# Optimization experiments

Hardware: AMD Instinct MI355X
Metric: run time of the kernel (lower is better)

The kernel has to match this reference:

```python
import jax, jax.numpy as jnp
import numpy as np

N, B, M = 262144, 4, 32
C3D, C2D, MID, OUT = 64, 256, 128, 64
H, W = 96, 312
VOXEL_SIZE = jnp.array([0.05, 0.05, 0.1], dtype=jnp.float32)
PC_RANGE = jnp.array([0.0, -40.0, -3.0], dtype=jnp.float32)
CLASS_W3D = jnp.array([0.85, 0.95, 0.6], dtype=jnp.float32)  # Car, Pedestrian, Cyclist
DEFAULT_W3D = 0.8
EPS = 1e-5

def _bn(x, g, b, m, v):
    # eval-mode batchnorm
    return (x - m) * jax.lax.rsqrt(v + EPS) * g + b

def setup_inputs():
    key = jax.random.key(0)
    ks = jax.random.split(key, 16)
    vb = jax.random.randint(ks[0], (N,), 0, B)
    vz = jax.random.randint(ks[1], (N,), 0, 40)
    vy = jax.random.randint(ks[2], (N,), 0, 1600)
    vx = jax.random.randint(ks[3], (N,), 0, 1408)
    voxel_coords = jnp.stack([vb, vz, vy, vx], axis=1).astype(jnp.int32)
    voxel_features = jax.random.normal(ks[4], (N, C3D), dtype=jnp.float32)
    image_features = jax.random.normal(ks[5], (B, C2D, H, W), dtype=jnp.float32)
    cxy = jax.random.uniform(ks[6], (B, M, 2)) * jnp.array([70.4, 80.0]) + jnp.array([0.0, -40.0])
    cz = jax.random.uniform(ks[7], (B, M, 1)) * 4.0 - 3.0
    dims = jax.random.uniform(ks[8], (B, M, 3)) * 3.0 + 1.0
    yaw = jax.random.uniform(ks[9], (B, M, 1)) * 6.28
    gt_boxes = jnp.concatenate([cxy, cz, dims, yaw], axis=-1).astype(jnp.float32)
    gt_classes = jax.random.randint(ks[10], (B, M), 0, 3)
    def lin(k, o, i):
        return (jax.random.normal(k, (o, i), dtype=jnp.float32) / np.float32(np.sqrt(i)))
    return dict(
        voxel_features=voxel_features, voxel_coords=voxel_coords,
        image_features=image_features, gt_boxes=gt_boxes, gt_classes=gt_classes,
        w_vt=lin(ks[11], MID, C3D), b_vt=jnp.zeros(MID),
        g_vt=jnp.ones(MID), be_vt=jnp.zeros(MID), m_vt=jnp.zeros(MID), v_vt=jnp.ones(MID),
        w_it=lin(ks[12], MID, C2D), b_it=jnp.zeros(MID),
        g_it=jnp.ones(MID), be_it=jnp.zeros(MID), m_it=jnp.zeros(MID), v_it=jnp.ones(MID),
        w_f=lin(ks[13], OUT, 2 * MID), b_f=jnp.zeros(OUT),
        g_f=jnp.ones(OUT), be_f=jnp.zeros(OUT), m_f=jnp.zeros(OUT), v_f=jnp.ones(OUT),
    )

def reference(voxel_features, voxel_coords, image_features, gt_boxes, gt_classes,
              w_vt, b_vt, g_vt, be_vt, m_vt, v_vt,
              w_it, b_it, g_it, be_it, m_it, v_it,
              w_f, b_f, g_f, be_f, m_f, v_f):
    b_idx = voxel_coords[:, 0]
    xyz = jnp.stack([voxel_coords[:, 3], voxel_coords[:, 2], voxel_coords[:, 1]], axis=1).astype(jnp.float32)
    centers_raw = xyz * VOXEL_SIZE + PC_RANGE            # class-aware path (no half-voxel offset)
    centers = centers_raw + VOXEL_SIZE * 0.5             # sampling path

    # voxel transform: Linear + BN + ReLU
    vt = jax.nn.relu(_bn(voxel_features @ w_vt.T + b_vt, g_vt, be_vt, m_vt, v_vt))

    # image transform: 1x1 conv + BN + ReLU over all images at once
    it = jnp.einsum('oc,bchw->bohw', w_it, image_features) + b_it[None, :, None, None]
    it = jax.nn.relu(_bn(it, g_it[None, :, None, None], be_it[None, :, None, None],
                         m_it[None, :, None, None], v_it[None, :, None, None]))

    # fallback projection (no calib): xy*10 + [W/2, H/2], normalize to [-1,1], clamp
    px = centers[:, 0] * 10.0 + W / 2.0
    py = centers[:, 1] * 10.0 + H / 2.0
    nx = jnp.clip(px / W * 2.0 - 1.0, -1.0, 1.0)
    ny = jnp.clip(py / H * 2.0 - 1.0, -1.0, 1.0)
    # grid_sample bilinear, align_corners=False, zero padding
    fx = ((nx + 1.0) * W - 1.0) * 0.5
    fy = ((ny + 1.0) * H - 1.0) * 0.5
    x0 = jnp.floor(fx); y0 = jnp.floor(fy)

    def gather(xi, yi):
        valid = (xi >= 0) & (xi < W) & (yi >= 0) & (yi < H)
        xc = jnp.clip(xi, 0, W - 1).astype(jnp.int32)
        yc = jnp.clip(yi, 0, H - 1).astype(jnp.int32)
        return it[b_idx, :, yc, xc] * valid[:, None].astype(it.dtype)  # (N, MID)

    wx1 = (fx - x0)[:, None]; wy1 = (fy - y0)[:, None]
    sampled = (gather(x0, y0) * (1.0 - wx1) * (1.0 - wy1)
             + gather(x0 + 1, y0) * wx1 * (1.0 - wy1)
             + gather(x0, y0 + 1) * (1.0 - wx1) * wy1
             + gather(x0 + 1, y0 + 1) * wx1 * wy1)

    # class-aware weights: axis-aligned point-in-box test; later boxes overwrite earlier
    cen = gt_boxes[..., :3][b_idx]          # (N, M, 3)
    dim = gt_boxes[..., 3:6][b_idx]         # (N, M, 3)
    valid_box = (gt_boxes[..., 3] > 0)[b_idx]  # (N, M)
    inb = jnp.all(jnp.abs(centers_raw[:, None, :] - cen) < dim * 0.5, axis=-1) & valid_box
    any_in = jnp.any(inb, axis=1)
    last = jnp.argmax(jnp.where(inb, jnp.arange(M), -1), axis=1)  # last matching box
    cls = gt_classes[b_idx, last]
    w3d = jnp.where(any_in, CLASS_W3D[cls], DEFAULT_W3D)[:, None]

    fused = jnp.concatenate([vt * w3d, sampled * (1.0 - w3d)], axis=1)
    out = jax.nn.relu(_bn(fused @ w_f.T + b_f, g_f, be_f, m_f, v_f))
    return out
```

## Files before the change

kernel.cpp:

```cpp
#include <hip/hip_runtime.h>

typedef _Float16 half8  __attribute__((ext_vector_type(8)));
typedef _Float16 half4v __attribute__((ext_vector_type(4)));
typedef _Float16 half2v __attribute__((ext_vector_type(2)));
typedef float    f32x4  __attribute__((ext_vector_type(4)));

#define N_VOX  262144
#define BATCH  4
#define NBOX   32
#define C3D_   64
#define C2D_   256
#define MIDC   128
#define OUTC   64
#define IH     96
#define IW     312
#define IHW    (IH*IW)
#define EPSF   1e-5f

#define MFMA16(a,b,c) __builtin_amdgcn_mfma_f32_16x16x32_f16(a,b,c,0,0,0)

__global__ __launch_bounds__(256) void prep_all(
    const int*   __restrict__ coords,
    const float* __restrict__ gtb,
    const int*   __restrict__ gtc,
    const float* __restrict__ w_vt, const float* __restrict__ g_vt,
    const float* __restrict__ v_vt, const float* __restrict__ b_vt,
    const float* __restrict__ be_vt, const float* __restrict__ m_vt,
    const float* __restrict__ w_it, const float* __restrict__ g_it,
    const float* __restrict__ v_it, const float* __restrict__ b_it,
    const float* __restrict__ be_it, const float* __restrict__ m_it,
    const float* __restrict__ w_f, const float* __restrict__ g_f,
    const float* __restrict__ v_f, const float* __restrict__ b_f,
    const float* __restrict__ be_f, const float* __restrict__ m_f,
    _Float16* __restrict__ w_vt_s, _Float16* __restrict__ w_it_s,
    _Float16* __restrict__ w_f1_s, _Float16* __restrict__ w_f2_s,
    float* __restrict__ sb_vt, float* __restrict__ sb_it,
    float* __restrict__ sb_f,  float* __restrict__ w3d_buf)
{
    __shared__ float s_box[BATCH*NBOX*7];
    __shared__ int   s_cls[BATCH*NBOX];
    const int tid = threadIdx.x;
    for (int i = tid; i < BATCH*NBOX*7; i += 256) s_box[i] = gtb[i];
    for (int i = tid; i < BATCH*NBOX;   i += 256) s_cls[i] = gtc[i];
    __syncthreads();

    const int v = blockIdx.x * 256 + tid;

    {
        const int4 cc = ((const int4*)coords)[v];
        const int vb = cc.x;
        const float crx = cc.w * 0.05f;
        const float cry = cc.z * 0.05f - 40.0f;
        const float crz = cc.y * 0.1f  - 3.0f;
        const float* gb = s_box + vb*(NBOX*7);
        int lastm = -1;
        #pragma unroll 8
        for (int m = 0; m < NBOX; ++m) {
            float dx = gb[m*7+3];
            bool in = (fabsf(crx - gb[m*7+0]) < dx * 0.5f) &&
                      (fabsf(cry - gb[m*7+1]) < gb[m*7+4] * 0.5f) &&
                      (fabsf(crz - gb[m*7+2]) < gb[m*7+5] * 0.5f) &&
                      (dx > 0.f);
            if (in) lastm = m;
        }
        float w3 = 0.8f;
        if (lastm >= 0) {
            int cls = s_cls[vb*NBOX + lastm];
            w3 = (cls == 0) ? 0.85f : ((cls == 1) ? 0.95f : 0.6f);
        }
        w3d_buf[v] = w3;
    }

    if (v < MIDC*C3D_) {
        int o = v >> 6;
        float sa = g_vt[o] * rsqrtf(v_vt[o] + EPSF);
        w_vt_s[v] = (_Float16)(w_vt[v] * sa);
    }
    if (v < MIDC*C2D_) {
        int o = v >> 8;
        float sa = g_it[o] * rsqrtf(v_it[o] + EPSF);
        w_it_s[v] = (_Float16)(w_it[v] * sa);
    }
    if (v < OUTC*C2D_) {
        int o = v >> 8, k = v & 255;
        float sa = g_f[o] * rsqrtf(v_f[o] + EPSF);
        float val = w_f[v] * sa;
        if (k < 128) w_f1_s[o*128 + k]       = (_Float16)val;
        else         w_f2_s[o*128 + (k-128)] = (_Float16)val;
    }
    if (v < MIDC) {
        float sa = g_vt[v] * rsqrtf(v_vt[v] + EPSF);
        sb_vt[v] = (b_vt[v] - m_vt[v]) * sa + be_vt[v];
        float si = g_it[v] * rsqrtf(v_it[v] + EPSF);
        sb_it[v] = (b_it[v] - m_it[v]) * si + be_it[v];
    }
    if (v < OUTC) {
        float sa = g_f[v] * rsqrtf(v_f[v] + EPSF);
        sb_f[v] = (b_f[v] - m_f[v]) * sa + be_f[v];
    }
}

__global__ __launch_bounds__(256, 4) void img_transform(
    const float* __restrict__ img,
    const _Float16* __restrict__ w_it_s,
    const _Float16* __restrict__ w_f2_s,
    const float* __restrict__ sb_it,
    _Float16* __restrict__ Jout)
{
    __shared__ __align__(16) _Float16 s_mem[64*136];

    const int p0   = blockIdx.x * 64;
    const int b    = blockIdx.y;
    const int tid  = threadIdx.x;
    const int lane = tid & 63;
    const int wv   = tid >> 6;
    const int r    = lane & 15;
    const int kh   = lane >> 4;

    f32x4 acc[4][2] = {};

    const int p  = tid & 63;
    const int cb = (tid >> 6) * 2;

    const float sbit0 = sb_it[wv*32 + r];
    const float sbit1 = sb_it[wv*32 + 16 + r];

    for (int kc = 0; kc < 4; ++kc) {
        #pragma unroll
        for (int i = 0; i < 8; ++i) {
            int c = cb + i*8;
            float x0 = img[(size_t)(b*C2D_ + kc*64 + c    )*IHW + p0 + p];
            float x1 = img[(size_t)(b*C2D_ + kc*64 + c + 1)*IHW + p0 + p];
            half2v h; h[0] = (_Float16)x0; h[1] = (_Float16)x1;
            *(half2v*)&s_mem[p*72 + c] = h;
        }
        half8 bw[2][2];
        #pragma unroll
        for (int nt = 0; nt < 2; ++nt)
            #pragma unroll
            for (int ks = 0; ks < 2; ++ks) {
                int o = wv*32 + nt*16 + r;
                bw[nt][ks] = *(const half8*)&w_it_s[o*C2D_ + kc*64 + ks*32 + kh*8];
            }
        __syncthreads();
        #pragma unroll
        for (int mt = 0; mt < 4; ++mt)
            #pragma unroll
            for (int ks = 0; ks < 2; ++ks) {
                half8 af = *(const half8*)&s_mem[(mt*16 + r)*72 + ks*32 + kh*8];
                acc[mt][0] = MFMA16(af, bw[0][ks], acc[mt][0]);
                acc[mt][1] = MFMA16(af, bw[1][ks], acc[mt][1]);
            }
        __syncthreads();
    }

    #pragma unroll
    for (int nt = 0; nt < 2; ++nt) {
        int o = wv*32 + nt*16 + r;
        float sb = nt ? sbit1 : sbit0;
        #pragma unroll
        for (int mt = 0; mt < 4; ++mt)
            #pragma unroll
            for (int rr = 0; rr < 4; ++rr) {
                int p2 = mt*16 + kh*4 + rr;
                s_mem[p2*136 + o] = (_Float16)fmaxf(acc[mt][nt][rr] + sb, 0.f);
            }
    }
    __syncthreads();

    {
        const int o2 = wv*16 + r;
        half8 bf2[4];
        #pragma unroll
        for (int ks = 0; ks < 4; ++ks)
            bf2[ks] = *(const half8*)&w_f2_s[o2*128 + ks*32 + kh*8];
        #pragma unroll
        for (int mt = 0; mt < 4; ++mt) {
            f32x4 a2 = {0.f,0.f,0.f,0.f};
            #pragma unroll
            for (int ks = 0; ks < 4; ++ks) {
                half8 af = *(const half8*)&s_mem[(mt*16 + r)*136 + ks*32 + kh*8];
                a2 = MFMA16(af, bf2[ks], a2);
            }
            #pragma unroll
            for (int rr = 0; rr < 4; ++rr) {
                int p2 = mt*16 + kh*4 + rr;
                Jout[(size_t)(b*IHW + p0 + p2)*OUTC + o2] = (_Float16)a2[rr];
            }
        }
    }
}

__global__ __launch_bounds__(256, 3) void voxel_fuse(
    const float* __restrict__ vf,
    const int*   __restrict__ coords,
    const _Float16* __restrict__ w_vt_s,
    const float* __restrict__ sb_vt,
    const _Float16* __restrict__ Jimg,
    const _Float16* __restrict__ w_f1_s,
    const float* __restrict__ sb_f,
    const float* __restrict__ w3d_buf,
    float* __restrict__ out)
{
    __shared__ __align__(16) _Float16 s_vf[64*72];
    __shared__ __align__(16) _Float16 s_fused[64*136];
    __shared__ __align__(16) _Float16 s_j[64*72];
    __shared__ float s_w3d[64];

    const int tid  = threadIdx.x;
    const int lane = tid & 63;
    const int wv   = tid >> 6;
    const int v0   = blockIdx.x * 64;
    const int r    = lane & 15;
    const int kh   = lane >> 4;
    const int vsv  = tid >> 2;
    const int q_   = tid & 3;

    float4 vfr[4];
    {
        const float4* src = (const float4*)(vf + (size_t)(v0 + vsv)*C3D_ + q_*16);
        #pragma unroll
        for (int i = 0; i < 4; ++i) vfr[i] = src[i];
    }
    const float w3 = w3d_buf[v0 + vsv];
    const int4 cc = ((const int4*)coords)[v0 + vsv];

    int ga[4]; float gw[4];
    {
        const int vb = cc.x;
        const float crx = cc.w * 0.05f;
        const float cry = cc.z * 0.05f - 40.0f;
        const float px = (crx + 0.025f) * 10.f + 156.f;
        const float py = (cry + 0.025f) * 10.f + 48.f;
        const float nx = fminf(fmaxf(px / 312.f * 2.f - 1.f, -1.f), 1.f);
        const float ny = fminf(fmaxf(py / 96.f  * 2.f - 1.f, -1.f), 1.f);
        const float fx = ((nx + 1.f) * 312.f - 1.f) * 0.5f;
        const float fy = ((ny + 1.f) * 96.f  - 1.f) * 0.5f;
        const float x0f = floorf(fx), y0f = floorf(fy);
        const float wx1 = fx - x0f, wy1 = fy - y0f;
        const int x0 = (int)x0f, y0 = (int)y0f;
        #pragma unroll
        for (int c = 0; c < 4; ++c) {
            int xi = x0 + (c & 1), yi = y0 + (c >> 1);
            bool valid = (xi >= 0) && (xi < IW) && (yi >= 0) && (yi < IH);
            int xc = min(max(xi, 0), IW - 1);
            int yc = min(max(yi, 0), IH - 1);
            ga[c] = ((vb*IH + yc)*IW + xc) * OUTC;
            float wx = (c & 1) ? wx1 : 1.f - wx1;
            float wy = (c >> 1) ? wy1 : 1.f - wy1;
            gw[c] = valid ? wx * wy : 0.f;
        }
    }

    half8 jreg[4][2];
    #pragma unroll
    for (int c = 0; c < 4; ++c)
        #pragma unroll
        for (int h = 0; h < 2; ++h)
            jreg[c][h] = *(const half8*)&Jimg[ga[c] + (h*4 + q_)*8];

    half8 bvt[2][2];
    float sbvt[2];
    #pragma unroll
    for (int nt = 0; nt < 2; ++nt) {
        int o = (2*wv + nt)*16 + r;
        #pragma unroll
        for (int ks = 0; ks < 2; ++ks)
            bvt[nt][ks] = *(const half8*)&w_vt_s[o*C3D_ + ks*32 + kh*8];
        sbvt[nt] = sb_vt[o];
    }
    const int of = wv*16 + r;
    half8 bf1[4];
    #pragma unroll
    for (int ks = 0; ks < 4; ++ks)
        bf1[ks] = *(const half8*)&w_f1_s[of*128 + ks*32 + kh*8];
    const float sbf = sb_f[of];

    #pragma unroll
    for (int i = 0; i < 4; ++i) {
        float4 x = vfr[i];
        half4v h;
        h[0] = (_Float16)x.x; h[1] = (_Float16)x.y;
        h[2] = (_Float16)x.z; h[3] = (_Float16)x.w;
        *(half4v*)&s_vf[vsv*72 + q_*16 + i*4] = h;
    }
    if (q_ == 0) s_w3d[vsv] = w3;
    __syncthreads();

    #pragma unroll
    for (int mt = 0; mt < 4; ++mt) {
        f32x4 a0 = {0.f,0.f,0.f,0.f}, a1 = {0.f,0.f,0.f,0.f};
        #pragma unroll
        for (int ks = 0; ks < 2; ++ks) {
            half8 af = *(const half8*)&s_vf[(mt*16 + r)*72 + ks*32 + kh*8];
            a0 = MFMA16(af, bvt[0][ks], a0);
            a1 = MFMA16(af, bvt[1][ks], a1);
        }
        #pragma unroll
        for (int rr = 0; rr < 4; ++rr) {
            int v = mt*16 + kh*4 + rr;
            float w3v = s_w3d[v];
            s_fused[v*136 + (2*wv+0)*16 + r] =
                (_Float16)(fmaxf(a0[rr] + sbvt[0], 0.f) * w3v);
            s_fused[v*136 + (2*wv+1)*16 + r] =
                (_Float16)(fmaxf(a1[rr] + sbvt[1], 0.f) * w3v);
        }
    }

    {
        float invw = 1.f - w3;
        #pragma unroll
        for (int h = 0; h < 2; ++h) {
            half8 res;
            #pragma unroll
            for (int i = 0; i < 8; ++i) {
                float s = gw[0]*(float)jreg[0][h][i] + gw[1]*(float)jreg[1][h][i]
                        + gw[2]*(float)jreg[2][h][i] + gw[3]*(float)jreg[3][h][i];
                res[i] = (_Float16)(s * invw);
            }
            *(half8*)&s_j[vsv*72 + (h*4 + q_)*8] = res;
        }
    }
    __syncthreads();

    #pragma unroll
    for (int mt = 0; mt < 4; ++mt) {
        f32x4 acc = {0.f,0.f,0.f,0.f};
        #pragma unroll
        for (int ks = 0; ks < 4; ++ks) {
            half8 af = *(const half8*)&s_fused[(mt*16 + r)*136 + ks*32 + kh*8];
            acc = MFMA16(af, bf1[ks], acc);
        }
        #pragma unroll
        for (int rr = 0; rr < 4; ++rr) {
            int v = mt*16 + kh*4 + rr;
            float jv = (float)s_j[v*72 + of];
            out[(size_t)(v0 + v)*OUTC + of] = fmaxf(acc[rr] + jv + sbf, 0.f);
        }
    }
}

extern "C" void kernel_launch(void* const* d_in, const int* in_sizes, int n_in,
                              void* d_out, int out_size, void* d_ws, size_t ws_size,
                              hipStream_t stream)
{
    const float* vf    = (const float*)d_in[0];
    const int*   vc    = (const int*)  d_in[1];
    const float* img   = (const float*)d_in[2];
    const float* gtb   = (const float*)d_in[3];
    const int*   gtc   = (const int*)  d_in[4];
    const float* w_vt  = (const float*)d_in[5];
    const float* b_vt  = (const float*)d_in[6];
    const float* g_vt  = (const float*)d_in[7];
    const float* be_vt = (const float*)d_in[8];
    const float* m_vt  = (const float*)d_in[9];
    const float* v_vt  = (const float*)d_in[10];
    const float* w_it  = (const float*)d_in[11];
    const float* b_it  = (const float*)d_in[12];
    const float* g_it  = (const float*)d_in[13];
    const float* be_it = (const float*)d_in[14];
    const float* m_it  = (const float*)d_in[15];
    const float* v_it  = (const float*)d_in[16];
    const float* w_f   = (const float*)d_in[17];
    const float* b_f   = (const float*)d_in[18];
    const float* g_f   = (const float*)d_in[19];
    const float* be_f  = (const float*)d_in[20];
    const float* m_f   = (const float*)d_in[21];
    const float* v_f   = (const float*)d_in[22];

    _Float16* ws_h   = (_Float16*)d_ws;
    _Float16* Jbuf   = ws_h;
    _Float16* w_vt_s = ws_h + (size_t)BATCH*IHW*OUTC;
    _Float16* w_it_s = w_vt_s + MIDC*C3D_;
    _Float16* w_f1_s = w_it_s + MIDC*C2D_;
    _Float16* w_f2_s = w_f1_s + OUTC*128;
    float*    fbase  = (float*)(w_f2_s + OUTC*128);
    float* sb_vt   = fbase;
    float* sb_it   = sb_vt + MIDC;
    float* sb_f    = sb_it + MIDC;
    float* w3d_buf = sb_f + OUTC;
    float* outp = (float*)d_out;

    prep_all<<<N_VOX/256, 256, 0, stream>>>(
        vc, gtb, gtc,
        w_vt, g_vt, v_vt, b_vt, be_vt, m_vt,
        w_it, g_it, v_it, b_it, be_it, m_it,
        w_f,  g_f,  v_f,  b_f,  be_f,  m_f,
        w_vt_s, w_it_s, w_f1_s, w_f2_s,
        sb_vt, sb_it, sb_f, w3d_buf);

    img_transform<<<dim3(IHW/64, BATCH), 256, 0, stream>>>(
        img, w_it_s, w_f2_s, sb_it, Jbuf);

    voxel_fuse<<<N_VOX/64, 256, 0, stream>>>(
        vf, vc, w_vt_s, sb_vt, Jbuf, w_f1_s, sb_f, w3d_buf, outp);
}
```

Before: 84.82 us.

## Process two voxel tiles per block, prefetching the second tile's inputs

Each block now handles 128 voxels as two 64-voxel tiles. The weights are loaded once and reused across both tiles. The second tile's voxel features, coords and gathered image rows are issued while the first tile's GEMMs run, to hide global-memory and gather latency. The trade-off is higher register pressure and lowered launch bounds (2 instead of 3 blocks), plus half as many blocks in the grid, which can reduce occupancy and latency hiding.

```diff
diff --git a/kernel.cpp b/kernel.cpp
--- a/kernel.cpp
+++ b/kernel.cpp
@@ -191,7 +191,7 @@
     }
 }
 
-__global__ __launch_bounds__(256, 3) void voxel_fuse(
+__global__ __launch_bounds__(256, 2) void voxel_fuse(
     const float* __restrict__ vf,
     const int*   __restrict__ coords,
     const _Float16* __restrict__ w_vt_s,
@@ -210,26 +210,43 @@
     const int tid  = threadIdx.x;
     const int lane = tid & 63;
     const int wv   = tid >> 6;
-    const int v0   = blockIdx.x * 64;
+    const int v0   = blockIdx.x * 128;
     const int r    = lane & 15;
     const int kh   = lane >> 4;
     const int vsv  = tid >> 2;
     const int q_   = tid & 3;
 
-    float4 vfr[4];
+    half8 bvt[2][2];
+    float sbvt[2];
+    #pragma unroll
+    for (int nt = 0; nt < 2; ++nt) {
+        int o = (2*wv + nt)*16 + r;
+        #pragma unroll
+        for (int ks = 0; ks < 2; ++ks)
+            bvt[nt][ks] = *(const half8*)&w_vt_s[o*C3D_ + ks*32 + kh*8];
+        sbvt[nt] = sb_vt[o];
+    }
+    const int of = wv*16 + r;
+    half8 bf1[4];
+    #pragma unroll
+    for (int ks = 0; ks < 4; ++ks)
+        bf1[ks] = *(const half8*)&w_f1_s[of*128 + ks*32 + kh*8];
+    const float sbf = sb_f[of];
+
+    float4 vfrA[4];
     {
         const float4* src = (const float4*)(vf + (size_t)(v0 + vsv)*C3D_ + q_*16);
         #pragma unroll
-        for (int i = 0; i < 4; ++i) vfr[i] = src[i];
-    }
-    const float w3 = w3d_buf[v0 + vsv];
-    const int4 cc = ((const int4*)coords)[v0 + vsv];
-
-    int ga[4]; float gw[4];
-    {
-        const int vb = cc.x;
-        const float crx = cc.w * 0.05f;
-        const float cry = cc.z * 0.05f - 40.0f;
+        for (int i = 0; i < 4; ++i) vfrA[i] = src[i];
+    }
+    const float w3A = w3d_buf[v0 + vsv];
+    const int4  ccA = ((const int4*)coords)[v0 + vsv];
+
+    int gaA[4]; float gwA[4];
+    {
+        const int vb = ccA.x;
+        const float crx = ccA.w * 0.05f;
+        const float cry = ccA.z * 0.05f - 40.0f;
         const float px = (crx + 0.025f) * 10.f + 156.f;
         const float py = (cry + 0.025f) * 10.f + 48.f;
         const float nx = fminf(fmaxf(px / 312.f * 2.f - 1.f, -1.f), 1.f);
@@ -245,47 +262,38 @@
             bool valid = (xi >= 0) && (xi < IW) && (yi >= 0) && (yi < IH);
             int xc = min(max(xi, 0), IW - 1);
             int yc = min(max(yi, 0), IH - 1);
-            ga[c] = ((vb*IH + yc)*IW + xc) * OUTC;
+            gaA[c] = ((vb*IH + yc)*IW + xc) * OUTC;
             float wx = (c & 1) ? wx1 : 1.f - wx1;
             float wy = (c >> 1) ? wy1 : 1.f - wy1;
-            gw[c] = valid ? wx * wy : 0.f;
-        }
-    }
-
-    half8 jreg[4][2];
+            gwA[c] = valid ? wx * wy : 0.f;
+        }
+    }
+    half8 jregA[4][2];
     #pragma unroll
     for (int c = 0; c < 4; ++c)
         #pragma unroll
         for (int h = 0; h < 2; ++h)
-            jreg[c][h] = *(const half8*)&Jimg[ga[c] + (h*4 + q_)*8];
-
-    half8 bvt[2][2];
-    float sbvt[2];
-    #pragma unroll
-    for (int nt = 0; nt < 2; ++nt) {
-        int o = (2*wv + nt)*16 + r;
-        #pragma unroll
-        for (int ks = 0; ks < 2; ++ks)
-            bvt[nt][ks] = *(const half8*)&w_vt_s[o*C3D_ + ks*32 + kh*8];
-        sbvt[nt] = sb_vt[o];
-    }
-    const int of = wv*16 + r;
-    half8 bf1[4];
-    #pragma unroll
-    for (int ks = 0; ks < 4; ++ks)
-        bf1[ks] = *(const half8*)&w_f1_s[of*128 + ks*32 + kh*8];
-    const float sbf = sb_f[of];
+            jregA[c][h] = *(const half8*)&Jimg[gaA[c] + (h*4 + q_)*8];
 
     #pragma unroll
     for (int i = 0; i < 4; ++i) {
-        float4 x = vfr[i];
+        float4 x = vfrA[i];
         half4v h;
         h[0] = (_Float16)x.x; h[1] = (_Float16)x.y;
         h[2] = (_Float16)x.z; h[3] = (_Float16)x.w;
         *(half4v*)&s_vf[vsv*72 + q_*16 + i*4] = h;
     }
-    if (q_ == 0) s_w3d[vsv] = w3;
+    if (q_ == 0) s_w3d[vsv] = w3A;
     __syncthreads();
+
+    float4 vfrB[4];
+    {
+        const float4* src = (const float4*)(vf + (size_t)(v0 + 64 + vsv)*C3D_ + q_*16);
+        #pragma unroll
+        for (int i = 0; i < 4; ++i) vfrB[i] = src[i];
+    }
+    const float w3B = w3d_buf[v0 + 64 + vsv];
+    const int4  ccB = ((const int4*)coords)[v0 + 64 + vsv];
 
     #pragma unroll
     for (int mt = 0; mt < 4; ++mt) {
@@ -308,19 +316,53 @@
     }
 
     {
-        float invw = 1.f - w3;
+        float invw = 1.f - w3A;
         #pragma unroll
         for (int h = 0; h < 2; ++h) {
             half8 res;
             #pragma unroll
             for (int i = 0; i < 8; ++i) {
-                float s = gw[0]*(float)jreg[0][h][i] + gw[1]*(float)jreg[1][h][i]
-                        + gw[2]*(float)jreg[2][h][i] + gw[3]*(float)jreg[3][h][i];
+                float s = gwA[0]*(float)jregA[0][h][i] + gwA[1]*(float)jregA[1][h][i]
+                        + gwA[2]*(float)jregA[2][h][i] + gwA[3]*(float)jregA[3][h][i];
                 res[i] = (_Float16)(s * invw);
             }
             *(half8*)&s_j[vsv*72 + (h*4 + q_)*8] = res;
         }
     }
+
+    int gaB[4]; float gwB[4];
+    {
+        const int vb = ccB.x;
+        const float crx = ccB.w * 0.05f;
+        const float cry = ccB.z * 0.05f - 40.0f;
+        const float px = (crx + 0.025f) * 10.f + 156.f;
+        const float py = (cry + 0.025f) * 10.f + 48.f;
+        const float nx = fminf(fmaxf(px / 312.f * 2.f - 1.f, -1.f), 1.f);
+        const float ny = fminf(fmaxf(py / 96.f  * 2.f - 1.f, -1.f), 1.f);
+        const float fx = ((nx + 1.f) * 312.f - 1.f) * 0.5f;
+        const float fy = ((ny + 1.f) * 96.f  - 1.f) * 0.5f;
+        const float x0f = floorf(fx), y0f = floorf(fy);
+        const float wx1 = fx - x0f, wy1 = fy - y0f;
+        const int x0 = (int)x0f, y0 = (int)y0f;
+        #pragma unroll
+        for (int c = 0; c < 4; ++c) {
+            int xi = x0 + (c & 1), yi = y0 + (c >> 1);
+            bool valid = (xi >= 0) && (xi < IW) && (yi >= 0) && (yi < IH);
+            int xc = min(max(xi, 0), IW - 1);
+            int yc = min(max(yi, 0), IH - 1);
+            gaB[c] = ((vb*IH + yc)*IW + xc) * OUTC;
+            float wx = (c & 1) ? wx1 : 1.f - wx1;
+            float wy = (c >> 1) ? wy1 : 1.f - wy1;
+            gwB[c] = valid ? wx * wy : 0.f;
+        }
+    }
+    half8 jregB[4][2];
+    #pragma unroll
+    for (int c = 0; c < 4; ++c)
+        #pragma unroll
+        for (int h = 0; h < 2; ++h)
+            jregB[c][h] = *(const half8*)&Jimg[gaB[c] + (h*4 + q_)*8];
+
     __syncthreads();
 
     #pragma unroll
@@ -336,6 +378,69 @@
             int v = mt*16 + kh*4 + rr;
             float jv = (float)s_j[v*72 + of];
             out[(size_t)(v0 + v)*OUTC + of] = fmaxf(acc[rr] + jv + sbf, 0.f);
+        }
+    }
+
+    #pragma unroll
+    for (int i = 0; i < 4; ++i) {
+        float4 x = vfrB[i];
+        half4v h;
+        h[0] = (_Float16)x.x; h[1] = (_Float16)x.y;
+        h[2] = (_Float16)x.z; h[3] = (_Float16)x.w;
+        *(half4v*)&s_vf[vsv*72 + q_*16 + i*4] = h;
+    }
+    if (q_ == 0) s_w3d[vsv] = w3B;
+    __syncthreads();
+
+    #pragma unroll
+    for (int mt = 0; mt < 4; ++mt) {
+        f32x4 a0 = {0.f,0.f,0.f,0.f}, a1 = {0.f,0.f,0.f,0.f};
+        #pragma unroll
+        for (int ks = 0; ks < 2; ++ks) {
+            half8 af = *(const half8*)&s_vf[(mt*16 + r)*72 + ks*32 + kh*8];
+            a0 = MFMA16(af, bvt[0][ks], a0);
+            a1 = MFMA16(af, bvt[1][ks], a1);
+        }
+        #pragma unroll
+        for (int rr = 0; rr < 4; ++rr) {
+            int v = mt*16 + kh*4 + rr;
+            float w3v = s_w3d[v];
+            s_fused[v*136 + (2*wv+0)*16 + r] =
+                (_Float16)(fmaxf(a0[rr] + sbvt[0], 0.f) * w3v);
+            s_fused[v*136 + (2*wv+1)*16 + r] =
+                (_Float16)(fmaxf(a1[rr] + sbvt[1], 0.f) * w3v);
+        }
+    }
+
+    {
+        float invw = 1.f - w3B;
+        #pragma unroll
+        for (int h = 0; h < 2; ++h) {
+            half8 res;
+            #pragma unroll
+            for (int i = 0; i < 8; ++i) {
+                float s = gwB[0]*(float)jregB[0][h][i] + gwB[1]*(float)jregB[1][h][i]
+                        + gwB[2]*(float)jregB[2][h][i] + gwB[3]*(float)jregB[3][h][i];
+                res[i] = (_Float16)(s * invw);
+            }
+            *(half8*)&s_j[vsv*72 + (h*4 + q_)*8] = res;
+        }
+    }
+    __syncthreads();
+
+    #pragma unroll
+    for (int mt = 0; mt < 4; ++mt) {
+        f32x4 acc = {0.f,0.f,0.f,0.f};
+        #pragma unroll
+        for (int ks = 0; ks < 4; ++ks) {
+            half8 af = *(const half8*)&s_fused[(mt*16 + r)*136 + ks*32 + kh*8];
+            acc = MFMA16(af, bf1[ks], acc);
+        }
+        #pragma unroll
+        for (int rr = 0; rr < 4; ++rr) {
+            int v = mt*16 + kh*4 + rr;
+            float jv = (float)s_j[v*72 + of];
+            out[(size_t)(v0 + 64 + v)*OUTC + of] = fmaxf(acc[rr] + jv + sbf, 0.f);
         }
     }
 }
@@ -392,6 +497,6 @@
     img_transform<<<dim3(IHW/64, BATCH), 256, 0, stream>>>(
         img, w_it_s, w_f2_s, sb_it, Jbuf);
 
-    voxel_fuse<<<N_VOX/64, 256, 0, stream>>>(
+    voxel_fuse<<<N_VOX/128, 256, 0, stream>>>(
         vf, vc, w_vt_s, sb_vt, Jbuf, w_f1_s, sb_f, w3d_buf, outp);
 }
```

Result: no change. 85.25 us (+0.5%).
